# Performance work log

Hardware: AMD Instinct MI355X
Metric: run time of the kernel (lower is better)

Reference implementation:

```python
import jax, jax.numpy as jnp
import numpy as np

LN_EPS = 1e-5  # torch LayerNorm default
K_NN = 5       # top-5 nearest patterns (simple-surprise path)


def setup_inputs() -> dict:
    key = jax.random.key(0)
    ks = jax.random.split(key, 5)
    B, S, D, M = 8, 8192, 256, 50
    return {
        "hidden_states": jax.random.normal(ks[0], (B, S, D), dtype=jnp.float32),
        "memory": jax.random.normal(ks[1], (M, D), dtype=jnp.float32),
        "W1": jax.random.normal(ks[2], (D, 2 * D), dtype=jnp.float32) * (1.0 / np.sqrt(D)),
        "b1": jnp.zeros((2 * D,), dtype=jnp.float32),
        "W2": jax.random.normal(ks[3], (2 * D, D), dtype=jnp.float32) * (1.0 / np.sqrt(2 * D)),
        "b2": jnp.zeros((D,), dtype=jnp.float32),
        "ln_gamma": jnp.ones((D,), dtype=jnp.float32),
        "ln_beta": jnp.zeros((D,), dtype=jnp.float32),
    }


def reference(hidden_states, memory, W1, b1, W2, b2, ln_gamma, ln_beta):
    # Feature extractor: Linear -> ReLU -> (Dropout, eval=identity) -> Linear -> LayerNorm
    h = jax.nn.relu(jnp.einsum("bsd,de->bse", hidden_states, W1) + b1)
    f = jnp.einsum("bse,ed->bsd", h, W2) + b2
    mu = jnp.mean(f, axis=-1, keepdims=True)
    var = jnp.var(f, axis=-1, keepdims=True)
    feats = (f - mu) * jax.lax.rsqrt(var + LN_EPS) * ln_gamma + ln_beta  # [B,S,D]

    # Simple-surprise path, vectorized over all (b, s) tokens:
    # L2 distance of each token feature to every memory pattern.
    f_sq = jnp.sum(feats * feats, axis=-1)      # [B,S]
    m_sq = jnp.sum(memory * memory, axis=-1)    # [M]
    dots = jnp.einsum("bsd,md->bsm", feats, memory)  # [B,S,M]
    d2 = jnp.maximum(f_sq[..., None] + m_sq - 2.0 * dots, 0.0)
    dists = jnp.sqrt(d2)                        # [B,S,M]

    # k smallest distances -> mean -> sigmoid(avg - 1)
    neg_knn, _ = jax.lax.top_k(-dists, K_NN)    # [B,S,K]
    avg_dist = -jnp.mean(neg_knn, axis=-1)      # [B,S]
    surprise_scores = jax.nn.sigmoid(avg_dist - 1.0)
    return surprise_scores
```

## Files before the change

kernel.cpp:

```cpp
#include <hip/hip_runtime.h>
#include <math.h>

typedef __attribute__((ext_vector_type(8))) short bf16x8;
typedef __attribute__((ext_vector_type(4))) float f32x4;

static __device__ __forceinline__ unsigned short f2b(float x) {
  unsigned int u = __float_as_uint(x);
  u += 0x7FFFu + ((u >> 16) & 1u);
  return (unsigned short)(u >> 16);
}

__global__ void prep_weights(const float* __restrict__ W1,
                             const float* __restrict__ W2,
                             const float* __restrict__ mem,
                             unsigned short* __restrict__ W1T,
                             unsigned short* __restrict__ W2T,
                             unsigned short* __restrict__ memB) {
  int i = blockIdx.x * 256 + threadIdx.x;
  if (i < 131072) {
    int k = i >> 9, n = i & 511;
    W1T[n * 256 + k] = f2b(W1[i]);
  } else if (i < 262144) {
    int j = i - 131072;
    int k = j >> 8, n = j & 255;
    W2T[n * 512 + k] = f2b(W2[j]);
  } else if (i < 278528) {
    int j = i - 262144;
    int r = j >> 8;
    memB[j] = (r < 50) ? f2b(mem[j]) : (unsigned short)0;
  }
}

__global__ void prep_msq(const float* __restrict__ mem, float* __restrict__ msq) {
  int r = blockIdx.x;
  float s = 0.f;
  if (r < 50) {
    for (int c = threadIdx.x; c < 256; c += 64) {
      float v = mem[r * 256 + c];
      s += v * v;
    }
  }
  for (int m = 1; m < 64; m <<= 1) s += __shfl_xor(s, m, 64);
  if (threadIdx.x == 0) msq[r] = (r < 50) ? s : 1e30f;
}

#define XP 264
#define HP 136
#define DPitch 65

__global__ __launch_bounds__(256, 3) void fused_main(
    const float* __restrict__ X, const float* __restrict__ b1v,
    const float* __restrict__ b2v, const float* __restrict__ gammav,
    const float* __restrict__ betav, const unsigned short* __restrict__ W1T,
    const unsigned short* __restrict__ W2T,
    const unsigned short* __restrict__ memB, const float* __restrict__ msq,
    float* __restrict__ out) {
  __shared__ __align__(16) char smem[54272];
  unsigned short* Xs = (unsigned short*)smem;
  unsigned short* Hs = (unsigned short*)(smem + 33792);
  float* distS = (float*)(smem + 33792);
  float* red = (float*)(smem + 50432);
  float* psum   = red;
  float* psumsq = red + 256;
  float* fsqp   = red + 512;
  float* muS    = red + 768;
  float* rstdS  = red + 832;
  float* fsqS   = red + 896;

  const int tid = threadIdx.x;
  const int wid = tid >> 6;
  const int lane = tid & 63;
  const int l16 = lane & 15;
  const int quad = lane >> 4;

  const float4* X4 = (const float4*)(X + (size_t)blockIdx.x * 64 * 256);
#pragma unroll
  for (int j = 0; j < 16; ++j) {
    int idx = j * 256 + tid;
    float4 v = X4[idx];
    int row = idx >> 6, c4 = (idx & 63) << 2;
    unsigned int p0 = f2b(v.x) | ((unsigned int)f2b(v.y) << 16);
    unsigned int p1 = f2b(v.z) | ((unsigned int)f2b(v.w) << 16);
    *(uint2*)(&Xs[row * XP + c4]) = make_uint2(p0, p1);
  }

  f32x4 acc2[4][4];
#pragma unroll
  for (int mt = 0; mt < 4; ++mt) {
    const float4 bb = *(const float4*)(&b2v[wid * 64 + mt * 16 + quad * 4]);
#pragma unroll
    for (int nt = 0; nt < 4; ++nt) {
      acc2[mt][nt][0] = bb.x; acc2[mt][nt][1] = bb.y;
      acc2[mt][nt][2] = bb.z; acc2[mt][nt][3] = bb.w;
    }
  }

  __syncthreads();

  for (int cc = 0; cc < 4; ++cc) {
    int hbase = cc * 128 + wid * 32;
    f32x4 acc1[2][4];
#pragma unroll
    for (int mt = 0; mt < 2; ++mt) {
      const float4 bb = *(const float4*)(&b1v[hbase + mt * 16 + quad * 4]);
#pragma unroll
      for (int nt = 0; nt < 4; ++nt) {
        acc1[mt][nt][0] = bb.x; acc1[mt][nt][1] = bb.y;
        acc1[mt][nt][2] = bb.z; acc1[mt][nt][3] = bb.w;
      }
    }
#pragma unroll
    for (int kk = 0; kk < 8; ++kk) {
      int k0 = kk * 32 + quad * 8;
      bf16x8 a[2], b[4];
#pragma unroll
      for (int mt = 0; mt < 2; ++mt)
        a[mt] = *(const bf16x8*)(W1T + (hbase + mt * 16 + l16) * 256 + k0);
#pragma unroll
      for (int nt = 0; nt < 4; ++nt)
        b[nt] = *(const bf16x8*)(Xs + (nt * 16 + l16) * XP + k0);
#pragma unroll
      for (int mt = 0; mt < 2; ++mt)
#pragma unroll
        for (int nt = 0; nt < 4; ++nt)
          acc1[mt][nt] = __builtin_amdgcn_mfma_f32_16x16x32_bf16(
              a[mt], b[nt], acc1[mt][nt], 0, 0, 0);
    }
    __syncthreads();
#pragma unroll
    for (int mt = 0; mt < 2; ++mt) {
#pragma unroll
      for (int nt = 0; nt < 4; ++nt) {
        int token = nt * 16 + l16;
        int hloc = wid * 32 + mt * 16 + quad * 4;
        f32x4 v = acc1[mt][nt];
        unsigned int p0 = f2b(fmaxf(v[0], 0.f)) | ((unsigned int)f2b(fmaxf(v[1], 0.f)) << 16);
        unsigned int p1 = f2b(fmaxf(v[2], 0.f)) | ((unsigned int)f2b(fmaxf(v[3], 0.f)) << 16);
        *(uint2*)(&Hs[token * HP + hloc]) = make_uint2(p0, p1);
      }
    }
    __syncthreads();
#pragma unroll
    for (int k2 = 0; k2 < 4; ++k2) {
      int k0 = k2 * 32 + quad * 8;
      bf16x8 a[4], b[4];
#pragma unroll
      for (int mt = 0; mt < 4; ++mt)
        a[mt] = *(const bf16x8*)(W2T + (wid * 64 + mt * 16 + l16) * 512 + cc * 128 + k0);
#pragma unroll
      for (int nt = 0; nt < 4; ++nt)
        b[nt] = *(const bf16x8*)(Hs + (nt * 16 + l16) * HP + k0);
#pragma unroll
      for (int mt = 0; mt < 4; ++mt)
#pragma unroll
        for (int nt = 0; nt < 4; ++nt)
          acc2[mt][nt] = __builtin_amdgcn_mfma_f32_16x16x32_bf16(
              a[mt], b[nt], acc2[mt][nt], 0, 0, 0);
    }
  }

  __syncthreads();

#pragma unroll
  for (int nt = 0; nt < 4; ++nt) {
    float s = 0.f, sq = 0.f;
#pragma unroll
    for (int mt = 0; mt < 4; ++mt)
#pragma unroll
      for (int r = 0; r < 4; ++r) {
        float v = acc2[mt][nt][r];
        s += v; sq += v * v;
      }
    s += __shfl_xor(s, 16, 64); sq += __shfl_xor(sq, 16, 64);
    s += __shfl_xor(s, 32, 64); sq += __shfl_xor(sq, 32, 64);
    if (quad == 0) {
      psum[wid * 64 + nt * 16 + l16] = s;
      psumsq[wid * 64 + nt * 16 + l16] = sq;
    }
  }
  __syncthreads();
  if (tid < 64) {
    float s = psum[tid] + psum[64 + tid] + psum[128 + tid] + psum[192 + tid];
    float sq = psumsq[tid] + psumsq[64 + tid] + psumsq[128 + tid] + psumsq[192 + tid];
    float mu = s * (1.f / 256.f);
    float var = sq * (1.f / 256.f) - mu * mu;
    muS[tid] = mu;
    rstdS[tid] = rsqrtf(var + 1e-5f);
  }
  __syncthreads();

  {
    float4 g[4], be[4];
#pragma unroll
    for (int mt = 0; mt < 4; ++mt) {
      g[mt]  = *(const float4*)(&gammav[wid * 64 + mt * 16 + quad * 4]);
      be[mt] = *(const float4*)(&betav[wid * 64 + mt * 16 + quad * 4]);
    }
#pragma unroll
    for (int nt = 0; nt < 4; ++nt) {
      int token = nt * 16 + l16;
      float mu = muS[token], rs = rstdS[token];
      float fs = 0.f;
#pragma unroll
      for (int mt = 0; mt < 4; ++mt) {
        float y0 = (acc2[mt][nt][0] - mu) * rs * g[mt].x + be[mt].x;
        float y1 = (acc2[mt][nt][1] - mu) * rs * g[mt].y + be[mt].y;
        float y2 = (acc2[mt][nt][2] - mu) * rs * g[mt].z + be[mt].z;
        float y3 = (acc2[mt][nt][3] - mu) * rs * g[mt].w + be[mt].w;
        fs += y0 * y0 + y1 * y1 + y2 * y2 + y3 * y3;
        unsigned int p0 = f2b(y0) | ((unsigned int)f2b(y1) << 16);
        unsigned int p1 = f2b(y2) | ((unsigned int)f2b(y3) << 16);
        *(uint2*)(&Xs[token * XP + wid * 64 + mt * 16 + quad * 4]) =
            make_uint2(p0, p1);
      }
      fs += __shfl_xor(fs, 16, 64);
      fs += __shfl_xor(fs, 32, 64);
      if (quad == 0) fsqp[wid * 64 + token] = fs;
    }
  }
  __syncthreads();
  if (tid < 64)
    fsqS[tid] = fsqp[tid] + fsqp[64 + tid] + fsqp[128 + tid] + fsqp[192 + tid];
  __syncthreads();

  f32x4 acc3[4];
#pragma unroll
  for (int nt = 0; nt < 4; ++nt) {
    acc3[nt][0] = 0.f; acc3[nt][1] = 0.f; acc3[nt][2] = 0.f; acc3[nt][3] = 0.f;
  }
#pragma unroll
  for (int kk = 0; kk < 8; ++kk) {
    int k0 = kk * 32 + quad * 8;
    bf16x8 a = *(const bf16x8*)(Xs + (wid * 16 + l16) * XP + k0);
#pragma unroll
    for (int nt = 0; nt < 4; ++nt) {
      bf16x8 b = *(const bf16x8*)(memB + (nt * 16 + l16) * 256 + k0);
      acc3[nt] = __builtin_amdgcn_mfma_f32_16x16x32_bf16(a, b, acc3[nt], 0, 0, 0);
    }
  }
  {
    float4 fsq4 = *(const float4*)(&fsqS[wid * 16 + quad * 4]);
#pragma unroll
    for (int nt = 0; nt < 4; ++nt) {
      int col = nt * 16 + l16;
      float mq = msq[col];
#pragma unroll
      for (int r = 0; r < 4; ++r) {
        float fv = (r == 0) ? fsq4.x : (r == 1) ? fsq4.y : (r == 2) ? fsq4.z : fsq4.w;
        float d2 = fv + mq - 2.f * acc3[nt][r];
        float d = sqrtf(fmaxf(d2, 0.f));
        int row = wid * 16 + quad * 4 + r;
        distS[row * DPitch + col] = d;
      }
    }
  }
  __syncthreads();

  if (tid < 64) {
    float b0 = 1e30f, b1 = 1e30f, b2 = 1e30f, b3 = 1e30f, b4 = 1e30f;
    const float* dr = &distS[tid * DPitch];
    for (int j = 0; j < 50; ++j) {
      float v = dr[j];
      b4 = fminf(b4, v);
      float t;
      if (b4 < b3) { t = b3; b3 = b4; b4 = t; }
      if (b3 < b2) { t = b2; b2 = b3; b3 = t; }
      if (b2 < b1) { t = b1; b1 = b2; b2 = t; }
      if (b1 < b0) { t = b0; b0 = b1; b1 = t; }
    }
    float avg = (b0 + b1 + b2 + b3 + b4) * 0.2f;
    float sarg = avg - 1.f;
    out[blockIdx.x * 64 + tid] = 1.f / (1.f + __expf(-sarg));
  }
}

extern "C" void kernel_launch(void* const* d_in, const int* in_sizes, int n_in,
                              void* d_out, int out_size, void* d_ws, size_t ws_size,
                              hipStream_t stream) {
  const float* X   = (const float*)d_in[0];
  const float* mem = (const float*)d_in[1];
  const float* W1  = (const float*)d_in[2];
  const float* b1  = (const float*)d_in[3];
  const float* W2  = (const float*)d_in[4];
  const float* b2  = (const float*)d_in[5];
  const float* g   = (const float*)d_in[6];
  const float* be  = (const float*)d_in[7];
  float* out = (float*)d_out;

  unsigned short* W1T  = (unsigned short*)d_ws;
  unsigned short* W2T  = W1T + 131072;
  unsigned short* memB = W2T + 131072;
  float* msq = (float*)(memB + 16384);

  prep_weights<<<1088, 256, 0, stream>>>(W1, W2, mem, W1T, W2T, memB);
  prep_msq<<<64, 64, 0, stream>>>(mem, msq);
  fused_main<<<1024, 256, 0, stream>>>(X, b1, b2, g, be, W1T, W2T, memB, msq, out);
}
```

Measured before the change: 196.6 us.

## Fold msq prep into weight prep, prefetch W2 tiles, shrink distance LDS

The separate msq kernel is merged into an extra block of prep_weights, which removes one launch. In fused_main, the first two k-steps of W2T fragments for each chunk are loaded before the GEMM1 loop so their global latency overlaps GEMM1 compute. The distance tile pitch drops from 65 to 53 and only the 50 valid columns are written, which shrinks shared memory. The prefetch costs extra VGPRs under the 3-blocks-per-CU launch bound, which risks spills or reduced occupancy.

```diff
diff --git a/kernel.cpp b/kernel.cpp
--- a/kernel.cpp
+++ b/kernel.cpp
@@ -15,7 +15,8 @@
                              const float* __restrict__ mem,
                              unsigned short* __restrict__ W1T,
                              unsigned short* __restrict__ W2T,
-                             unsigned short* __restrict__ memB) {
+                             unsigned short* __restrict__ memB,
+                             float* __restrict__ msq) {
   int i = blockIdx.x * 256 + threadIdx.x;
   if (i < 131072) {
     int k = i >> 9, n = i & 511;
@@ -28,25 +29,25 @@
     int j = i - 262144;
     int r = j >> 8;
     memB[j] = (r < 50) ? f2b(mem[j]) : (unsigned short)0;
-  }
-}
-
-__global__ void prep_msq(const float* __restrict__ mem, float* __restrict__ msq) {
-  int r = blockIdx.x;
-  float s = 0.f;
-  if (r < 50) {
-    for (int c = threadIdx.x; c < 256; c += 64) {
-      float v = mem[r * 256 + c];
-      s += v * v;
-    }
-  }
-  for (int m = 1; m < 64; m <<= 1) s += __shfl_xor(s, m, 64);
-  if (threadIdx.x == 0) msq[r] = (r < 50) ? s : 1e30f;
+  } else {
+    int t = threadIdx.x;
+    int r = t >> 2, c0 = (t & 3) * 64;
+    float s = 0.f;
+    if (r < 50) {
+      for (int c = 0; c < 64; ++c) {
+        float v = mem[r * 256 + c0 + c];
+        s += v * v;
+      }
+    }
+    s += __shfl_xor(s, 1, 64);
+    s += __shfl_xor(s, 2, 64);
+    if ((t & 3) == 0) msq[r] = (r < 50) ? s : 1e30f;
+  }
 }
 
 #define XP 264
 #define HP 136
-#define DPitch 65
+#define DPitch 53
 
 __global__ __launch_bounds__(256, 3) void fused_main(
     const float* __restrict__ X, const float* __restrict__ b1v,
@@ -55,11 +56,11 @@
     const unsigned short* __restrict__ W2T,
     const unsigned short* __restrict__ memB, const float* __restrict__ msq,
     float* __restrict__ out) {
-  __shared__ __align__(16) char smem[54272];
+  __shared__ __align__(16) char smem[51200];
   unsigned short* Xs = (unsigned short*)smem;
   unsigned short* Hs = (unsigned short*)(smem + 33792);
   float* distS = (float*)(smem + 33792);
-  float* red = (float*)(smem + 50432);
+  float* red = (float*)(smem + 47360);
   float* psum   = red;
   float* psumsq = red + 256;
   float* fsqp   = red + 512;
@@ -109,6 +110,13 @@
         acc1[mt][nt][2] = bb.z; acc1[mt][nt][3] = bb.w;
       }
     }
+    bf16x8 a2p[2][4];
+#pragma unroll
+    for (int k2 = 0; k2 < 2; ++k2)
+#pragma unroll
+      for (int mt = 0; mt < 4; ++mt)
+        a2p[k2][mt] = *(const bf16x8*)(W2T + (wid * 64 + mt * 16 + l16) * 512 +
+                                       cc * 128 + k2 * 32 + quad * 8);
 #pragma unroll
     for (int kk = 0; kk < 8; ++kk) {
       int k0 = kk * 32 + quad * 8;
@@ -145,8 +153,13 @@
       int k0 = k2 * 32 + quad * 8;
       bf16x8 a[4], b[4];
 #pragma unroll
-      for (int mt = 0; mt < 4; ++mt)
-        a[mt] = *(const bf16x8*)(W2T + (wid * 64 + mt * 16 + l16) * 512 + cc * 128 + k0);
+      for (int mt = 0; mt < 4; ++mt) {
+        if (k2 < 2)
+          a[mt] = a2p[k2][mt];
+        else
+          a[mt] = *(const bf16x8*)(W2T + (wid * 64 + mt * 16 + l16) * 512 +
+                                   cc * 128 + k0 - quad * 8 + quad * 8);
+      }
 #pragma unroll
       for (int nt = 0; nt < 4; ++nt)
         b[nt] = *(const bf16x8*)(Hs + (nt * 16 + l16) * HP + k0);
@@ -250,7 +263,7 @@
         float d2 = fv + mq - 2.f * acc3[nt][r];
         float d = sqrtf(fmaxf(d2, 0.f));
         int row = wid * 16 + quad * 4 + r;
-        distS[row * DPitch + col] = d;
+        if (col < 50) distS[row * DPitch + col] = d;
       }
     }
   }
@@ -292,7 +305,6 @@
   unsigned short* memB = W2T + 131072;
   float* msq = (float*)(memB + 16384);
 
-  prep_weights<<<1088, 256, 0, stream>>>(W1, W2, mem, W1T, W2T, memB);
-  prep_msq<<<64, 64, 0, stream>>>(mem, msq);
+  prep_weights<<<1089, 256, 0, stream>>>(W1, W2, mem, W1T, W2T, memB, msq);
   fused_main<<<1024, 256, 0, stream>>>(X, b1, b2, g, be, W1T, W2T, memB, msq, out);
 }
```

New measurement: 215.4 us. 9.6% more time.
